# Optimization experiments

Hardware: AMD Instinct MI355X
Metric: run time of the kernel (lower is better)

The kernel has to match this reference:

```python
import jax, jax.numpy as jnp
import numpy as np

B, S, H = 2, 2048, 2048
NH, NKV, HD = 16, 4, 128
GROUPS = NH // NKV
THETA = 10000.0
EPS = 1e-6


def setup_inputs() -> dict:
    key = jax.random.key(0)
    ks = jax.random.split(key, 6)
    scale = 0.02
    return {
        "hidden_states": jax.random.normal(ks[0], (B, S, H), jnp.float32),
        "wq": jax.random.normal(ks[1], (NH * HD, H), jnp.float32) * scale,
        "wk": jax.random.normal(ks[2], (NKV * HD, H), jnp.float32) * scale,
        "wv": jax.random.normal(ks[3], (NKV * HD, H), jnp.float32) * scale,
        "wo": jax.random.normal(ks[4], (H, NH * HD), jnp.float32) * scale,
        "q_norm_weight": jnp.ones((HD,), jnp.float32),
        "k_norm_weight": jnp.ones((HD,), jnp.float32),
    }


def _rope_tables(seq_len):
    inv_freq = 1.0 / (THETA ** (jnp.arange(0, HD, 2, dtype=jnp.float32) / HD))
    t = jnp.arange(seq_len, dtype=jnp.float32)
    freqs = jnp.outer(t, inv_freq)              # [S, HD/2]
    emb = jnp.concatenate([freqs, freqs], -1)   # [S, HD]
    return jnp.cos(emb), jnp.sin(emb)


def _rotate_half(x):
    x1, x2 = x[..., : HD // 2], x[..., HD // 2:]
    return jnp.concatenate([-x2, x1], -1)


def _rmsnorm(x, w):
    var = jnp.mean(jnp.square(x), axis=-1, keepdims=True)
    return x * jax.lax.rsqrt(var + EPS) * w


def reference(hidden_states, wq, wk, wv, wo, q_norm_weight, k_norm_weight):
    b, s, _ = hidden_states.shape
    q = (hidden_states @ wq.T).reshape(b, s, NH, HD).transpose(0, 2, 1, 3)    # [b,nh,s,d]
    k = (hidden_states @ wk.T).reshape(b, s, NKV, HD).transpose(0, 2, 1, 3)   # [b,nkv,s,d]
    v = (hidden_states @ wv.T).reshape(b, s, NKV, HD).transpose(0, 2, 1, 3)

    cos, sin = _rope_tables(s)                  # [s,d]
    q = q * cos + _rotate_half(q) * sin
    k = k * cos + _rotate_half(k) * sin

    # fused QK RMSNorm (applied inside fused_qknorm_flash_attention)
    q = _rmsnorm(q, q_norm_weight)
    k = _rmsnorm(k, k_norm_weight)

    # GQA: share each kv head across GROUPS query heads without materializing repeats
    qg = q.reshape(b, NKV, GROUPS, s, HD)
    scale = 1.0 / jnp.sqrt(jnp.float32(HD))
    scores = jnp.einsum('bhgqd,bhkd->bhgqk', qg, k) * scale   # [b,nkv,g,s,s]
    causal = jnp.tril(jnp.ones((s, s), bool))
    scores = jnp.where(causal, scores, jnp.finfo(scores.dtype).min)
    probs = jax.nn.softmax(scores, axis=-1)
    out = jnp.einsum('bhgqk,bhkd->bhgqd', probs, v)            # [b,nkv,g,s,d]
    out = out.reshape(b, NH, s, HD).transpose(0, 2, 1, 3).reshape(b, s, NH * HD)
    return out @ wo.T
```

## Files before the change

### kernel.cpp

```cpp
#include <hip/hip_runtime.h>
#include <math.h>

typedef __bf16 bf16;
typedef __bf16 bf16x8 __attribute__((ext_vector_type(8)));
typedef __bf16 bf16x4 __attribute__((ext_vector_type(4)));
typedef float f32x4 __attribute__((ext_vector_type(4)));

#define B_DIM 2
#define S_LEN 2048
#define H_DIM 2048
#define NH 16
#define NKV 4
#define HD 128

__device__ __forceinline__ void gl_lds16(const void* g, void* l) {
    __builtin_amdgcn_global_load_lds(
        (const __attribute__((address_space(1))) unsigned int*)g,
        (__attribute__((address_space(3))) unsigned int*)l, 16, 0, 0);
}

__device__ __forceinline__ void bar() {
    asm volatile("" ::: "memory");
    __builtin_amdgcn_s_barrier();
    asm volatile("" ::: "memory");
}

__global__ __launch_bounds__(256) void cast_all(const float* __restrict__ s0,
                                                const float* __restrict__ s1,
                                                const float* __restrict__ s2,
                                                const float* __restrict__ s3,
                                                const float* __restrict__ s4,
                                                bf16* __restrict__ dst) {
    const int i = blockIdx.x * 256 + threadIdx.x;
    const float* src;
    int off;
    if (i < 2097152)      { src = s0; off = 0; }
    else if (i < 3145728) { src = s1; off = 2097152; }
    else if (i < 3407872) { src = s2; off = 3145728; }
    else if (i < 3670016) { src = s3; off = 3407872; }
    else                  { src = s4; off = 3670016; }
    float4 f = ((const float4*)src)[i - off];
    bf16x4 o = { (bf16)f.x, (bf16)f.y, (bf16)f.z, (bf16)f.w };
    *(bf16x4*)(dst + (size_t)i * 4) = o;
}

template <typename OutT>
__global__ __launch_bounds__(512, 2) void gemm256(const bf16* __restrict__ A,
                                                  const bf16* __restrict__ Bt,
                                                  OutT* __restrict__ C,
                                                  int M, int N, int K) {
    __shared__ __align__(16) bf16 smem[65536];
    const int t = threadIdx.x, lane = t & 63, w = t >> 6;
    const int lr = lane & 15, quad = lane >> 4;
    const int nN = N >> 8;
    const int nwg = gridDim.x, chunk = nwg >> 3;
    const int bid = blockIdx.x;
    const int lid = (bid & 7) * chunk + (bid >> 3);
    const int m0 = (lid / nN) << 8, n0 = (lid % nN) << 8;
    const int mh_w = w >> 2;
    const int wn = (w & 3) << 6;
    const int nh_w = (w & 3) >> 1;
    const int rb = (w & 1) << 6;
    const int nK = K >> 6;

    const int ld0 = w * 2;
    const int lrow = lane >> 2;
    const int csrc = (lane & 3) ^ ((lane >> 3) & 3);
    const int swz = (lr >> 1) & 3;

    auto stA = [&](int ts, int mh) {
        if (ts < nK) {
            bf16* db = smem + (ts & 1) * 16384 + mh * 8192;
            const bf16* sp = A + (size_t)(m0 + mh * 128) * K + ts * 64;
#pragma unroll
            for (int i = 0; i < 2; i++) {
                const int ldi = ld0 + i, kb = ldi >> 3, rg = ldi & 7;
                gl_lds16(sp + (size_t)(rg * 16 + lrow) * K + kb * 32 + csrc * 8,
                         db + kb * 4096 + rg * 512);
            }
        }
    };
    auto stB = [&](int ts, int nh) {
        if (ts < nK) {
            bf16* db = smem + 32768 + (ts & 1) * 16384 + nh * 8192;
            const bf16* sp = Bt + (size_t)(n0 + nh * 128) * K + ts * 64;
#pragma unroll
            for (int i = 0; i < 2; i++) {
                const int ldi = ld0 + i, kb = ldi >> 3, rg = ldi & 7;
                gl_lds16(sp + (size_t)(rg * 16 + lrow) * K + kb * 32 + csrc * 8,
                         db + kb * 4096 + rg * 512);
            }
        }
    };

    f32x4 acc[8][4];
#pragma unroll
    for (int i = 0; i < 8; i++)
#pragma unroll
        for (int j = 0; j < 4; j++) acc[i][j] = (f32x4){0.f, 0.f, 0.f, 0.f};
    bf16x8 af[8], b0[4], b1[4];

    auto rdA = [&](int s, int fi0) {
        const bf16* bp = smem + s * 16384 + mh_w * 8192;
#pragma unroll
        for (int f = 0; f < 4; f++)
#pragma unroll
            for (int ks = 0; ks < 2; ks++)
                af[f * 2 + ks] = *(const bf16x8*)(bp + ks * 4096 +
                                                  ((fi0 + f) * 16 + lr) * 32 + (quad ^ swz) * 8);
    };
    auto rdB = [&](int s, int fj0, bf16x8* dst) {
        const bf16* bp = smem + 32768 + s * 16384 + nh_w * 8192;
#pragma unroll
        for (int f = 0; f < 2; f++)
#pragma unroll
            for (int ks = 0; ks < 2; ks++)
                dst[f * 2 + ks] = *(const bf16x8*)(bp + ks * 4096 +
                                                   (rb + (fj0 + f) * 16 + lr) * 32 + (quad ^ swz) * 8);
    };
    auto mm16 = [&](int fi0, int fj0, bf16x8* bb) {
        __builtin_amdgcn_s_setprio(1);
#pragma unroll
        for (int f = 0; f < 4; f++)
#pragma unroll
            for (int g = 0; g < 2; g++)
#pragma unroll
                for (int ks = 0; ks < 2; ks++)
                    acc[fi0 + f][fj0 + g] = __builtin_amdgcn_mfma_f32_16x16x32_bf16(
                        af[f * 2 + ks], bb[g * 2 + ks], acc[fi0 + f][fj0 + g], 0, 0, 0);
        __builtin_amdgcn_s_setprio(0);
    };

    stB(0, 0); stB(0, 1); stA(0, 0); stA(0, 1);
    stB(1, 0); stB(1, 1); stA(1, 0);
    asm volatile("s_waitcnt vmcnt(6)" ::: "memory");
    bar();

    for (int ts = 0; ts < nK; ++ts) {
        const int s = ts & 1;
        rdA(s, 0); rdB(s, 0, b0);
        stA(ts + 1, 1);
        bar();
        mm16(0, 0, b0);
        bar();
        rdB(s, 2, b1);
        bar();
        mm16(0, 2, b1);
        bar();
        rdA(s, 4);
        stB(ts + 2, 0);
        bar();
        mm16(4, 2, b1);
        bar();
        stB(ts + 2, 1);
        stA(ts + 2, 0);
        bar();
        mm16(4, 0, b0);
        if (ts + 2 < nK) asm volatile("s_waitcnt vmcnt(6)" ::: "memory");
        else             asm volatile("s_waitcnt vmcnt(0)" ::: "memory");
        bar();
    }
#pragma unroll
    for (int fi = 0; fi < 8; fi++) {
        const int m = m0 + mh_w * 128 + fi * 16 + quad * 4;
#pragma unroll
        for (int fj = 0; fj < 4; fj++) {
            const int n = n0 + wn + fj * 16 + lr;
#pragma unroll
            for (int r = 0; r < 4; r++)
                C[(size_t)(m + r) * N + n] = (OutT)acc[fi][fj][r];
        }
    }
}

__global__ __launch_bounds__(256) void rope_rms(const bf16* __restrict__ qkv,
                                                const float* __restrict__ qw,
                                                const float* __restrict__ kw,
                                                bf16* __restrict__ qb,
                                                bf16* __restrict__ kb,
                                                bf16* __restrict__ vt) {
    const int tok = blockIdx.x;
    const int b = tok >> 11, s = tok & (S_LEN - 1);
    const int lane = threadIdx.x & 63, w = threadIdx.x >> 6;
    const bf16* row = qkv + (size_t)tok * 3072;
    const float inv = expf(-(float)lane * (9.210340371976184f / 64.f));
    const float ang = (float)s * inv;
    float s_, c_;
    sincosf(ang, &s_, &c_);
    const float wq1 = qw[lane], wq2 = qw[lane + 64];
    const float wk1 = kw[lane], wk2 = kw[lane + 64];
    for (int u = w; u < 24; u += 4) {
        if (u < 16) {
            const float x1 = (float)row[u * 128 + lane], x2 = (float)row[u * 128 + 64 + lane];
            float y1 = x1 * c_ - x2 * s_;
            float y2 = x2 * c_ + x1 * s_;
            float ss = y1 * y1 + y2 * y2;
#pragma unroll
            for (int m = 1; m < 64; m <<= 1) ss += __shfl_xor(ss, m);
            const float r = rsqrtf(ss * (1.f / 128.f) + 1e-6f);
            size_t o = ((size_t)(b * NH + u) * S_LEN + s) * HD;
            qb[o + lane]      = (bf16)(y1 * r * wq1);
            qb[o + 64 + lane] = (bf16)(y2 * r * wq2);
        } else if (u < 20) {
            const int kh = u - 16;
            const float x1 = (float)row[2048 + kh * 128 + lane], x2 = (float)row[2048 + kh * 128 + 64 + lane];
            float y1 = x1 * c_ - x2 * s_;
            float y2 = x2 * c_ + x1 * s_;
            float ss = y1 * y1 + y2 * y2;
#pragma unroll
            for (int m = 1; m < 64; m <<= 1) ss += __shfl_xor(ss, m);
            const float r = rsqrtf(ss * (1.f / 128.f) + 1e-6f);
            size_t base = (size_t)(b * NKV + kh) * 16 * 16384;
            kb[base + (size_t)(lane >> 3) * 16384 + s * 8 + (lane & 7)]       = (bf16)(y1 * r * wk1);
            kb[base + (size_t)(8 + (lane >> 3)) * 16384 + s * 8 + (lane & 7)] = (bf16)(y2 * r * wk2);
        } else {
            const int vh = u - 20;
            const float x1 = (float)row[2560 + vh * 128 + lane], x2 = (float)row[2560 + vh * 128 + 64 + lane];
            const int m = s & 31;
            const int gi = (s >> 5) * 4 + ((m & 15) >> 2);
            const int el = ((m >> 4) << 2) | (m & 3);
            size_t base = ((size_t)(b * NKV + vh) * 256 + gi) * 1024 + el;
            vt[base + (size_t)lane * 8]        = (bf16)x1;
            vt[base + (size_t)(lane + 64) * 8] = (bf16)x2;
        }
    }
}

__global__ __launch_bounds__(256, 3) void flash(const bf16* __restrict__ qg,
                                                const bf16* __restrict__ kg,
                                                const bf16* __restrict__ vg,
                                                bf16* __restrict__ attn,
                                                float* __restrict__ part_o,
                                                float* __restrict__ part_l) {
    static const unsigned char QT[22] = {9,8,15,15,7,14,14,13,13,6,12,12,11,11,5,10,10,4,3,2,1,0};
    static const unsigned char CK[22] = {2,2,0,1,2,0,1,0,1,2,0,1,0,1,2,0,1,2,2,2,2,2};
    const int idx = blockIdx.x;
    const int g = idx >> 5, hb = idx & 31;
    const int qt = QT[g], ck = CK[g];
    const int h = hb & 15, b = hb >> 4;
    const int kvh = h >> 2;
    const int ktBeg = (ck == 1) ? (qt + 1) : 0;
    const int ktEnd = (ck == 0) ? (qt + 1) : (2 * qt + 2);
    const bf16* qh = qg + (size_t)(b * NH + h) * S_LEN * HD;
    const bf16* kh = kg + (size_t)(b * NKV + kvh) * (16 * 16384);
    const bf16* vh = vg + (size_t)(b * NKV + kvh) * (256 * 1024);
    __shared__ __align__(16) bf16 Ks[2][16 * 512];
    __shared__ __align__(16) bf16 Vs[8 * 1024];
    const int t = threadIdx.x, lane = t & 63, w = t >> 6, lr = lane & 15, quad = lane >> 4;
    const int row0 = qt * 128 + w * 32;
    bf16x8 qf[2][4];
#pragma unroll
    for (int mg = 0; mg < 2; mg++)
#pragma unroll
        for (int c = 0; c < 4; c++)
            qf[mg][c] = *(const bf16x8*)(qh + (size_t)(row0 + mg * 16 + lr) * HD + c * 32 + quad * 8);
    f32x4 o[2][8];
    f32x4 lacc[2];
#pragma unroll
    for (int mg = 0; mg < 2; mg++) {
        lacc[mg] = (f32x4){0.f, 0.f, 0.f, 0.f};
#pragma unroll
        for (int j = 0; j < 8; j++) o[mg][j] = (f32x4){0.f, 0.f, 0.f, 0.f};
    }
    const bf16 one = (bf16)1.0f;
    const bf16x8 ones8 = {one, one, one, one, one, one, one, one};
    const float C1 = 0.12751744f;
    const float C2 = -17.3123405f;

    auto stageK = [&](int kt_) {
        if (kt_ < ktEnd) {
            bf16* dst = Ks[kt_ & 1];
            const int kb = kt_ * 64;
#pragma unroll
            for (int i = 0; i < 4; i++) {
                const int dc = w * 4 + i;
                gl_lds16(kh + (size_t)dc * 16384 + (size_t)kb * 8 + lane * 8, dst + dc * 512);
            }
        }
    };
    auto stageV = [&](int kt_) {
#pragma unroll
        for (int i = 0; i < 2; i++) {
            const int c = w * 2 + i;
            const bf16* src = vh + (size_t)(8 * kt_ + c) * 1024 + lane * 8;
            gl_lds16(src, &Vs[c * 1024]);
            gl_lds16(src + 512, &Vs[c * 1024 + 512]);
        }
    };

    stageK(ktBeg);
    stageK(ktBeg + 1);
    __syncthreads();

    for (int kt = ktBeg; kt < ktEnd; ++kt) {
        const int kbase = kt * 64;
        const int cur = kt & 1;
        stageV(kt);
        f32x4 sacc[2][4];
#pragma unroll
        for (int mg = 0; mg < 2; mg++)
#pragma unroll
            for (int n = 0; n < 4; n++) sacc[mg][n] = (f32x4){0.f, 0.f, 0.f, 0.f};
#pragma unroll
        for (int n = 0; n < 4; n++)
#pragma unroll
            for (int c = 0; c < 4; c++) {
                bf16x8 kf = *(const bf16x8*)&Ks[cur][(c * 4 + quad) * 512 + (n * 16 + lr) * 8];
                sacc[0][n] = __builtin_amdgcn_mfma_f32_16x16x32_bf16(kf, qf[0][c], sacc[0][n], 0, 0, 0);
                sacc[1][n] = __builtin_amdgcn_mfma_f32_16x16x32_bf16(kf, qf[1][c], sacc[1][n], 0, 0, 0);
            }
        const bool diag = (kt >= 2 * qt);
        bf16x8 pT[2][2];
#pragma unroll
        for (int mg = 0; mg < 2; mg++) {
            const int qrow = row0 + mg * 16 + lr;
#pragma unroll
            for (int n = 0; n < 4; n++)
#pragma unroll
                for (int r = 0; r < 4; r++) {
                    float ev = exp2f(fmaf(sacc[mg][n][r], C1, C2));
                    if (diag) {
                        const int key = kbase + n * 16 + quad * 4 + r;
                        ev = (key <= qrow) ? ev : 0.f;
                    }
                    pT[mg][n >> 1][(n & 1) * 4 + r] = (bf16)ev;
                }
        }
        asm volatile("s_waitcnt vmcnt(0)" ::: "memory");
        bar();
        stageK(kt + 2);
#pragma unroll
        for (int k2 = 0; k2 < 2; k2++) {
#pragma unroll
            for (int j = 0; j < 8; j++) {
                bf16x8 vf = *(const bf16x8*)&Vs[(k2 * 4 + quad) * 1024 + (j * 16 + lr) * 8];
                o[0][j] = __builtin_amdgcn_mfma_f32_16x16x32_bf16(vf, pT[0][k2], o[0][j], 0, 0, 0);
                o[1][j] = __builtin_amdgcn_mfma_f32_16x16x32_bf16(vf, pT[1][k2], o[1][j], 0, 0, 0);
            }
            lacc[0] = __builtin_amdgcn_mfma_f32_16x16x32_bf16(ones8, pT[0][k2], lacc[0], 0, 0, 0);
            lacc[1] = __builtin_amdgcn_mfma_f32_16x16x32_bf16(ones8, pT[1][k2], lacc[1], 0, 0, 0);
        }
        bar();
    }
    if (ck == 2) {
#pragma unroll
        for (int mg = 0; mg < 2; mg++) {
            const float inv = 1.0f / lacc[mg][0];
            const int qrow = row0 + mg * 16 + lr;
            bf16* dst = attn + ((size_t)(b * S_LEN) + qrow) * (NH * HD) + h * HD + quad * 4;
#pragma unroll
            for (int j = 0; j < 8; j++) {
                bf16x4 st = { (bf16)(o[mg][j][0] * inv), (bf16)(o[mg][j][1] * inv),
                              (bf16)(o[mg][j][2] * inv), (bf16)(o[mg][j][3] * inv) };
                *(bf16x4*)(dst + j * 16) = st;
            }
        }
    } else {
        const int slot = ((b * NH + h) * 6 + (qt - 10)) * 2 + ck;
        float* po = part_o + (size_t)slot * 16384;
#pragma unroll
        for (int mg = 0; mg < 2; mg++) {
            const int row = w * 32 + mg * 16 + lr;
#pragma unroll
            for (int j = 0; j < 8; j++) {
                float4 st = { o[mg][j][0], o[mg][j][1], o[mg][j][2], o[mg][j][3] };
                *(float4*)(po + row * 128 + j * 16 + quad * 4) = st;
            }
            if (quad == 0) part_l[slot * 128 + row] = lacc[mg][0];
        }
    }
}

__global__ __launch_bounds__(256) void reduce_attn(const float* __restrict__ part_o,
                                                   const float* __restrict__ part_l,
                                                   bf16* __restrict__ attn) {
    const int blk = blockIdx.x;
    const int qt = (blk % 6) + 10;
    const int h = (blk / 6) & 15, b = blk / 96;
    const float* p0 = part_o + (size_t)(blk * 2 + 0) * 16384;
    const float* p1 = part_o + (size_t)(blk * 2 + 1) * 16384;
    const float* l0 = part_l + (blk * 2 + 0) * 128;
    const float* l1 = part_l + (blk * 2 + 1) * 128;
    const int t = threadIdx.x;
#pragma unroll
    for (int it = 0; it < 16; it++) {
        const int idx = it * 256 + t;
        const int row = idx >> 5, d4 = idx & 31;
        float4 a = ((const float4*)p0)[idx];
        float4 c = ((const float4*)p1)[idx];
        const float inv = 1.0f / (l0[row] + l1[row]);
        bf16x4 ov = { (bf16)((a.x + c.x) * inv), (bf16)((a.y + c.y) * inv),
                      (bf16)((a.z + c.z) * inv), (bf16)((a.w + c.w) * inv) };
        *(bf16x4*)(attn + ((size_t)(b * S_LEN) + qt * 128 + row) * (NH * HD) + h * HD + d4 * 4) = ov;
    }
}

extern "C" void kernel_launch(void* const* d_in, const int* in_sizes, int n_in,
                              void* d_out, int out_size, void* d_ws, size_t ws_size,
                              hipStream_t stream) {
    (void)in_sizes; (void)n_in; (void)out_size; (void)ws_size;
    const float* hs  = (const float*)d_in[0];
    const float* wq  = (const float*)d_in[1];
    const float* wk  = (const float*)d_in[2];
    const float* wv  = (const float*)d_in[3];
    const float* wo  = (const float*)d_in[4];
    const float* qnw = (const float*)d_in[5];
    const float* knw = (const float*)d_in[6];
    float* out = (float*)d_out;

    char* ws = (char*)d_ws;
    size_t off = 0;
    auto alloc = [&](size_t bytes) {
        void* p = ws + off;
        off += (bytes + 255) & ~(size_t)255;
        return p;
    };
    bf16* hs_bf   = (bf16*)alloc((size_t)4096 * 2048 * 2);
    bf16* wqkv_bf = (bf16*)alloc((size_t)3072 * 2048 * 2);
    bf16* wo_bf   = (bf16*)alloc((size_t)2048 * 2048 * 2);
    bf16* qkv_bf  = (bf16*)alloc((size_t)4096 * 3072 * 2);
    bf16* q_bf    = (bf16*)alloc((size_t)B_DIM * NH * S_LEN * HD * 2);
    bf16* k_bf    = (bf16*)alloc((size_t)B_DIM * NKV * S_LEN * HD * 2);
    bf16* vt_bf   = (bf16*)alloc((size_t)B_DIM * NKV * S_LEN * HD * 2);
    bf16* at_bf   = (bf16*)alloc((size_t)4096 * 2048 * 2);

    float* part_o = (float*)hs_bf;
    float* part_l = (float*)((char*)hs_bf + (size_t)384 * 16384 * 4);

    cast_all<<<18432, 256, 0, stream>>>(hs, wq, wk, wv, wo, hs_bf);
    gemm256<bf16><<<dim3(192), 512, 0, stream>>>(hs_bf, wqkv_bf, qkv_bf, 4096, 3072, 2048);
    rope_rms<<<4096, 256, 0, stream>>>(qkv_bf, qnw, knw, q_bf, k_bf, vt_bf);
    flash<<<dim3(704), 256, 0, stream>>>(q_bf, k_bf, vt_bf, at_bf, part_o, part_l);
    reduce_attn<<<dim3(192), 256, 0, stream>>>(part_o, part_l, at_bf);
    gemm256<float><<<dim3(128), 512, 0, stream>>>(at_bf, wo_bf, out, 4096, 2048, 2048);
}
```

Measured before the change: 323.6 us.

## Simplify GEMM main loop to one-ahead prefetch with full B fragment reads

The GEMM pipeline moves from a staggered two-stage-ahead prefetch with four barrier-separated quarter MMA blocks to a simpler scheme. Each iteration loads all B fragments once, issues the next tile's full A and B loads, and runs two half-tile MMA blocks, then waits for all outstanding loads. The goal is fewer barriers and fewer B fragment reloads from LDS, at the cost of less load/compute overlap because of the full vmcnt(0) wait every iteration and more registers held for B. The attention QK loop is also reordered so the MFMA chains interleave across output tiles.

```diff
diff --git a/kernel.cpp b/kernel.cpp
--- a/kernel.cpp
+++ b/kernel.cpp
@@ -98,7 +98,7 @@
     for (int i = 0; i < 8; i++)
 #pragma unroll
         for (int j = 0; j < 4; j++) acc[i][j] = (f32x4){0.f, 0.f, 0.f, 0.f};
-    bf16x8 af[8], b0[4], b1[4];
+    bf16x8 af[8], bfull[8];
 
     auto rdA = [&](int s, int fi0) {
         const bf16* bp = smem + s * 16384 + mh_w * 8192;
@@ -109,55 +109,44 @@
                 af[f * 2 + ks] = *(const bf16x8*)(bp + ks * 4096 +
                                                   ((fi0 + f) * 16 + lr) * 32 + (quad ^ swz) * 8);
     };
-    auto rdB = [&](int s, int fj0, bf16x8* dst) {
+    auto rdBall = [&](int s) {
         const bf16* bp = smem + 32768 + s * 16384 + nh_w * 8192;
 #pragma unroll
-        for (int f = 0; f < 2; f++)
+        for (int f = 0; f < 4; f++)
 #pragma unroll
             for (int ks = 0; ks < 2; ks++)
-                dst[f * 2 + ks] = *(const bf16x8*)(bp + ks * 4096 +
-                                                   (rb + (fj0 + f) * 16 + lr) * 32 + (quad ^ swz) * 8);
-    };
-    auto mm16 = [&](int fi0, int fj0, bf16x8* bb) {
+                bfull[f * 2 + ks] = *(const bf16x8*)(bp + ks * 4096 +
+                                                     (rb + f * 16 + lr) * 32 + (quad ^ swz) * 8);
+    };
+    auto mm32 = [&](int fi0) {
         __builtin_amdgcn_s_setprio(1);
 #pragma unroll
-        for (int f = 0; f < 4; f++)
-#pragma unroll
-            for (int g = 0; g < 2; g++)
-#pragma unroll
-                for (int ks = 0; ks < 2; ks++)
-                    acc[fi0 + f][fj0 + g] = __builtin_amdgcn_mfma_f32_16x16x32_bf16(
-                        af[f * 2 + ks], bb[g * 2 + ks], acc[fi0 + f][fj0 + g], 0, 0, 0);
+        for (int ks = 0; ks < 2; ks++)
+#pragma unroll
+            for (int f = 0; f < 4; f++)
+#pragma unroll
+                for (int g = 0; g < 4; g++)
+                    acc[fi0 + f][g] = __builtin_amdgcn_mfma_f32_16x16x32_bf16(
+                        af[f * 2 + ks], bfull[g * 2 + ks], acc[fi0 + f][g], 0, 0, 0);
         __builtin_amdgcn_s_setprio(0);
     };
 
     stB(0, 0); stB(0, 1); stA(0, 0); stA(0, 1);
-    stB(1, 0); stB(1, 1); stA(1, 0);
-    asm volatile("s_waitcnt vmcnt(6)" ::: "memory");
+    asm volatile("s_waitcnt vmcnt(0)" ::: "memory");
     bar();
 
     for (int ts = 0; ts < nK; ++ts) {
         const int s = ts & 1;
-        rdA(s, 0); rdB(s, 0, b0);
-        stA(ts + 1, 1);
-        bar();
-        mm16(0, 0, b0);
-        bar();
-        rdB(s, 2, b1);
-        bar();
-        mm16(0, 2, b1);
+        rdA(s, 0); rdBall(s);
+        stA(ts + 1, 0); stA(ts + 1, 1);
+        stB(ts + 1, 0); stB(ts + 1, 1);
+        bar();
+        mm32(0);
         bar();
         rdA(s, 4);
-        stB(ts + 2, 0);
-        bar();
-        mm16(4, 2, b1);
-        bar();
-        stB(ts + 2, 1);
-        stA(ts + 2, 0);
-        bar();
-        mm16(4, 0, b0);
-        if (ts + 2 < nK) asm volatile("s_waitcnt vmcnt(6)" ::: "memory");
-        else             asm volatile("s_waitcnt vmcnt(0)" ::: "memory");
+        bar();
+        mm32(4);
+        asm volatile("s_waitcnt vmcnt(0)" ::: "memory");
         bar();
     }
 #pragma unroll
@@ -302,9 +291,9 @@
 #pragma unroll
             for (int n = 0; n < 4; n++) sacc[mg][n] = (f32x4){0.f, 0.f, 0.f, 0.f};
 #pragma unroll
-        for (int n = 0; n < 4; n++)
-#pragma unroll
-            for (int c = 0; c < 4; c++) {
+        for (int c = 0; c < 4; c++)
+#pragma unroll
+            for (int n = 0; n < 4; n++) {
                 bf16x8 kf = *(const bf16x8*)&Ks[cur][(c * 4 + quad) * 512 + (n * 16 + lr) * 8];
                 sacc[0][n] = __builtin_amdgcn_mfma_f32_16x16x32_bf16(kf, qf[0][c], sacc[0][n], 0, 0, 0);
                 sacc[1][n] = __builtin_amdgcn_mfma_f32_16x16x32_bf16(kf, qf[1][c], sacc[1][n], 0, 0, 0);
```

After: 346.2 us. 7.0% more time.
